# Performance work log

Measured on AMD Instinct MI355X. Metric: run time of the kernel, lower is better.

Reference implementation:

```python
import jax, jax.numpy as jnp
import numpy as np

N, E, D, ED, G = 50000, 800000, 64, 32, 50


def setup_inputs() -> dict:
    key = jax.random.key(0)
    ks = jax.random.split(key, 24)
    s = 0.05
    inp = {
        "x": jax.random.normal(ks[0], (N, D), jnp.float32),
        "edge_attr": jax.random.normal(ks[1], (E, ED), jnp.float32),
        "edge_index": jax.random.randint(ks[2], (2, E), 0, N, jnp.int64),
    }
    i = 3
    for step in range(2):
        inp[f"fe{step}_W1"] = jax.random.normal(ks[i], (2 * D + ED, D), jnp.float32) * s; i += 1
        inp[f"fe{step}_b1"] = jnp.zeros((D,), jnp.float32)
        inp[f"fe{step}_W2"] = jax.random.normal(ks[i], (D, D), jnp.float32) * s; i += 1
        inp[f"fe{step}_b2"] = jnp.zeros((D,), jnp.float32)
        inp[f"lstm{step}_Wih"] = jax.random.normal(ks[i], (D, 4 * D), jnp.float32) * s; i += 1
        inp[f"lstm{step}_Whh"] = jax.random.normal(ks[i], (D, 4 * D), jnp.float32) * s; i += 1
        inp[f"lstm{step}_bih"] = jnp.zeros((4 * D,), jnp.float32)
        inp[f"lstm{step}_bhh"] = jnp.zeros((4 * D,), jnp.float32)
    inp["gm_W"] = jax.random.normal(ks[i], (D, G), jnp.float32) * s; i += 1
    inp["gm_b"] = jnp.zeros((G,), jnp.float32)
    inp["fm_W"] = jax.random.normal(ks[i], (D, G), jnp.float32) * s; i += 1
    inp["fm_b"] = jnp.zeros((G,), jnp.float32)
    return inp


def _mpn(x, edge_attr, src, dst, W1, b1, W2, b2):
    # x_i = x[dst] (target), x_j = x[src] (source); aggregate 'add' at dst
    m = jnp.concatenate([x[dst], x[src], edge_attr], axis=1)  # [E, 2D+ED]
    m = jax.nn.relu(m @ W1 + b1) @ W2 + b2                    # [E, D]
    return jax.ops.segment_sum(m, dst, num_segments=x.shape[0])


def _lstm_cell(inp, h, c, Wih, Whh, bih, bhh):
    gates = inp @ Wih + h @ Whh + (bih + bhh)  # [N, 4D], gate order i,f,g,o
    i, f, g, o = jnp.split(gates, 4, axis=1)
    c = jax.nn.sigmoid(f) * c + jax.nn.sigmoid(i) * jnp.tanh(g)
    h = jax.nn.sigmoid(o) * jnp.tanh(c)
    return h, c


def reference(x, edge_attr, edge_index,
              fe0_W1, fe0_b1, fe0_W2, fe0_b2,
              lstm0_Wih, lstm0_Whh, lstm0_bih, lstm0_bhh,
              fe1_W1, fe1_b1, fe1_W2, fe1_b2,
              lstm1_Wih, lstm1_Whh, lstm1_bih, lstm1_bhh,
              gm_W, gm_b, fm_W, fm_b):
    src, dst = edge_index[0], edge_index[1]
    c = jnp.zeros_like(x)
    fes = [(fe0_W1, fe0_b1, fe0_W2, fe0_b2), (fe1_W1, fe1_b1, fe1_W2, fe1_b2)]
    lstms = [(lstm0_Wih, lstm0_Whh, lstm0_bih, lstm0_bhh),
             (lstm1_Wih, lstm1_Whh, lstm1_bih, lstm1_bhh)]
    for step in range(2):
        a = _mpn(x, edge_attr, src, dst, *fes[step])
        # LSTMCell(input=x, (h=a, c=c)) as in the original forward
        x, c = _lstm_cell(x, a, c, *lstms[step])
    g = jax.nn.sigmoid(x @ gm_W + gm_b)   # [N, G]
    h_v_G = x @ fm_W + fm_b               # [N, G]
    return jnp.sum(g * h_v_G, axis=0)     # [G]
```

## Files before the change

kernel.cpp:

```cpp
#include <hip/hip_runtime.h>
#include <hip/hip_bf16.h>

using short8 = __attribute__((ext_vector_type(8))) short;
using f32x4  = __attribute__((ext_vector_type(4))) float;

#define KLP 136

__device__ __forceinline__ unsigned short f2bf(float f) {
  unsigned u = __float_as_uint(f);
  u += 0x7FFFu + ((u >> 16) & 1u);
  return (unsigned short)(u >> 16);
}
__device__ __forceinline__ unsigned pack2(float a, float b) {
  return (unsigned)f2bf(a) | ((unsigned)f2bf(b) << 16);
}
#if __has_builtin(__builtin_amdgcn_rcpf)
__device__ __forceinline__ float fast_rcp(float x) { return __builtin_amdgcn_rcpf(x); }
#else
__device__ __forceinline__ float fast_rcp(float x) { return 1.f / x; }
#endif
__device__ __forceinline__ float sigm(float x) { return fast_rcp(1.f + __expf(-x)); }
__device__ __forceinline__ float tanh_f(float x) { return fmaf(2.f, sigm(2.f * x), -1.f); }

__global__ __launch_bounds__(256) void prep_all(
    const float* __restrict__ x,
    const float* __restrict__ W1_0, const float* __restrict__ Wih0,
    const float* __restrict__ bih0, const float* __restrict__ bhh0,
    const float* __restrict__ W1_1, const float* __restrict__ Wih1,
    const float* __restrict__ bih1, const float* __restrict__ bhh1,
    const float* __restrict__ W2_0, const float* __restrict__ Whh0, const float* __restrict__ b2_0,
    const float* __restrict__ W2_1, const float* __restrict__ Whh1, const float* __restrict__ b2_1,
    const float* __restrict__ gmW, const float* __restrict__ fmW,
    unsigned short* __restrict__ W1T,
    unsigned short* __restrict__ WcT,
    float* __restrict__ bG,
    float* __restrict__ b2h,
    unsigned short* __restrict__ WrT,
    unsigned short* __restrict__ xb0,
    float* __restrict__ aggrH,
    int* __restrict__ histA,
    float* __restrict__ outZ, int nOut,
    int N)
{
  int t = blockIdx.x * 256 + threadIdx.x;

  const int R0 = 2 * 26880 + 8192;
  if (t < R0) {
    const int per = 26880;
    if (t >= 2 * per) {
      int r2 = t - 2 * per;
      int o = r2 >> 6, k = r2 & 63;
      float v = 0.f;
      if (o < 50) v = gmW[k * 50 + o];
      else if (o >= 64 && o < 114) v = fmW[k * 50 + (o - 64)];
      WrT[o * 64 + k] = f2bf(v);
      return;
    }
    int step = t / per, r = t % per;
    const float* W1  = step ? W1_1 : W1_0;
    const float* Wih = step ? Wih1 : Wih0;
    const float* bih = step ? bih1 : bih0;
    const float* bhh = step ? bhh1 : bhh0;
    if (r < 10240) {
      int o = r / 160, k = r % 160;
      W1T[step * 10240 + o * 160 + k] = f2bf(W1[k * 64 + o]);
    } else if (r < 26624) {
      int rr = r - 10240;
      int g = rr >> 6, k = rr & 63;
      WcT[step * 32768 + g * 128 + k] = f2bf(Wih[k * 256 + g]);
    } else {
      int g = r - 26624;
      bG[step * 256 + g] = bih[g] + bhh[g];
    }
    return;
  }
  t -= R0;

  const int R1 = 33280;
  if (t < R1) {
    if (t < 32768) {
      int step = t >> 14, r = t & 16383;
      int g = r >> 6, k = r & 63;
      const float* W2  = step ? W2_1 : W2_0;
      const float* Whh = step ? Whh1 : Whh0;
      float v = 0.f;
      for (int j = 0; j < 64; ++j) v = fmaf(W2[k * 64 + j], Whh[j * 256 + g], v);
      WcT[step * 32768 + g * 128 + 64 + k] = f2bf(v);
    } else {
      int r = t - 32768;
      int step = r >> 8, g = r & 255;
      const float* b2  = step ? b2_1 : b2_0;
      const float* Whh = step ? Whh1 : Whh0;
      float v = 0.f;
      for (int j = 0; j < 64; ++j) v = fmaf(b2[j], Whh[j * 256 + g], v);
      b2h[step * 256 + g] = v;
    }
    return;
  }
  t -= R1;

  const int R2 = N * 8;
  if (t < R2) {
    const float4* p = (const float4*)(x + (long long)t * 8);
    float4 a0 = p[0], a1 = p[1];
    *(uint4*)(xb0 + (long long)t * 8) =
        make_uint4(pack2(a0.x, a0.y), pack2(a0.z, a0.w), pack2(a1.x, a1.y), pack2(a1.z, a1.w));
    return;
  }
  t -= R2;

  const int R3 = N * 16;
  if (t < R3) { ((float4*)aggrH)[t] = make_float4(0.f, 0.f, 0.f, 0.f); return; }
  t -= R3;

  const int R4 = N / 4;
  if (t < R4) { ((int4*)histA)[t] = make_int4(0, 0, 0, 0); return; }
  t -= R4;

  if (t < nOut) outZ[t] = 0.f;
}

__global__ __launch_bounds__(256) void hist_kernel(
    const int* __restrict__ dstI, int* __restrict__ hist, int E)
{
  int e = blockIdx.x * 256 + threadIdx.x;
  if (e < E) atomicAdd(&hist[dstI[e]], 1);
}

__global__ __launch_bounds__(256) void scan_part(
    const int* __restrict__ hist, int2* __restrict__ blockTot, int N)
{
  __shared__ int sD[256], sS[256];
  int t = threadIdx.x;
  int n = blockIdx.x * 256 + t;
  int d = (n < N) ? hist[n] : 0;
  int sg = (d + 15) >> 4;
  sD[t] = d; sS[t] = sg;
  __syncthreads();
  #pragma unroll
  for (int off = 128; off; off >>= 1) {
    if (t < off) { sD[t] += sD[t + off]; sS[t] += sS[t + off]; }
    __syncthreads();
  }
  if (t == 0) blockTot[blockIdx.x] = make_int2(sD[0], sS[0]);
}

__global__ __launch_bounds__(256) void scan_mid(
    const int2* __restrict__ blockTot, int2* __restrict__ blockBase,
    int* __restrict__ nSegTot, int nb)
{
  __shared__ int sD[256], sS[256];
  int t = threadIdx.x;
  int d = 0, s = 0;
  if (t < nb) { int2 v = blockTot[t]; d = v.x; s = v.y; }
  sD[t] = d; sS[t] = s;
  __syncthreads();
  #pragma unroll
  for (int off = 1; off < 256; off <<= 1) {
    int vd = (t >= off) ? sD[t - off] : 0;
    int vs = (t >= off) ? sS[t - off] : 0;
    __syncthreads();
    sD[t] += vd; sS[t] += vs;
    __syncthreads();
  }
  if (t < nb) blockBase[t] = make_int2(sD[t] - d, sS[t] - s);
  if (t == nb - 1) *nSegTot = sS[t];
}

__global__ __launch_bounds__(256) void scan_final(
    const int* __restrict__ hist, const int2* __restrict__ blockBase,
    int* __restrict__ cursor, int4* __restrict__ segInfo, int N)
{
  __shared__ int sD[256], sS[256];
  int t = threadIdx.x;
  int n = blockIdx.x * 256 + t;
  int d = (n < N) ? hist[n] : 0;
  int sg = (d + 15) >> 4;
  sD[t] = d; sS[t] = sg;
  __syncthreads();
  #pragma unroll
  for (int off = 1; off < 256; off <<= 1) {
    int vd = (t >= off) ? sD[t - off] : 0;
    int vs = (t >= off) ? sS[t - off] : 0;
    __syncthreads();
    sD[t] += vd; sS[t] += vs;
    __syncthreads();
  }
  if (n < N) {
    int2 bb = blockBase[blockIdx.x];
    int degBase = bb.x + sD[t] - d;
    int segBase = bb.y + sS[t] - sg;
    cursor[n] = degBase;
    for (int j = 0; j < sg; ++j)
      segInfo[segBase + j] = make_int4(degBase + j * 16, n, min(d - j * 16, 16), 0);
  }
}

__global__ __launch_bounds__(256) void scatter_perm(
    const int* __restrict__ srcI, const int* __restrict__ dstI,
    const float* __restrict__ ea, int* __restrict__ cursor,
    int* __restrict__ srcS, unsigned short* __restrict__ eaS, int E)
{
  const int t = threadIdx.x;
  const int l = t & 63;
  const int e = blockIdx.x * 64 + (t >> 2);
  const int c = t & 3;
  if (e >= E) return;
  int p = 0;
  if (c == 0) {
    int d = dstI[e];
    p = atomicAdd(&cursor[d], 1);
    srcS[p] = srcI[e];
  }
  p = __shfl(p, l & ~3);
  const float4* pe = (const float4*)(ea + (long long)e * 32 + c * 8);
  float4 a0 = pe[0], a1 = pe[1];
  *(uint4*)(eaS + (long long)p * 32 + c * 8) =
      make_uint4(pack2(a0.x, a0.y), pack2(a0.z, a0.w), pack2(a1.x, a1.y), pack2(a1.z, a1.w));
}

__global__ __launch_bounds__(256) void edge_gemm(
    const unsigned short* __restrict__ xb,
    const unsigned short* __restrict__ eaS,
    const int* __restrict__ srcS,
    const int4* __restrict__ segInfo,
    const int* __restrict__ nSegPtr,
    const unsigned short* __restrict__ W1T,
    const float* __restrict__ b1,
    float* __restrict__ aggrH)
{
  __shared__ unsigned short stash[20 * 64 * 8];
  const int t = threadIdx.x;
  const int w = t >> 6, l = t & 63;
  const int quad = l >> 4, lr = l & 15;

  #pragma unroll
  for (int p = 0; p < 5; ++p) {
    int idx = p * 256 + t;
    int grp = idx >> 6, ll = idx & 63;
    int kc = grp >> 2, n = grp & 3;
    *(uint4*)(stash + idx * 8) =
        *(const uint4*)(W1T + (n * 16 + (ll & 15)) * 160 + kc * 32 + (ll >> 4) * 8);
  }
  float bb[4];
  #pragma unroll
  for (int n = 0; n < 4; ++n) bb[n] = b1[n * 16 + lr];
  __syncthreads();

  const int nSeg = *nSegPtr;
  const int W = gridDim.x * 4;
  int s = blockIdx.x * 4 + w;
  if (s >= nSeg) return;
  int4 si = segInfo[s];
  int src = srcS[si.x + min(lr, si.z - 1)];

  while (true) {
    const int sn = s + W;
    const bool more = sn < nSeg;
    int4 si_n = si;
    if (more) si_n = segInfo[sn];

    const int start = si.x, node = si.y, cnt = si.z;
    const int er = min(lr, cnt - 1);

    const short8* pd = (const short8*)(xb + (long long)node * 64);
    const short8* ps = (const short8*)(xb + (long long)src * 64);
    short8 a0 = pd[quad];
    short8 a1 = pd[4 + quad];
    short8 a2 = ps[quad];
    short8 a3 = ps[4 + quad];
    short8 a4 = *(const short8*)(eaS + (long long)(start + er) * 32 + quad * 8);

    int src_n = src;
    if (more) src_n = srcS[si_n.x + min(lr, si_n.z - 1)];

    f32x4 acc[4] = {};
    #pragma unroll
    for (int kc = 0; kc < 5; ++kc) {
      short8 aX = (kc == 0) ? a0 : (kc == 1) ? a1 : (kc == 2) ? a2 : (kc == 3) ? a3 : a4;
      #pragma unroll
      for (int n = 0; n < 4; ++n) {
        short8 bFr = *(const short8*)(stash + (((kc << 2) | n) * 64 + l) * 8);
        acc[n] = __builtin_amdgcn_mfma_f32_16x16x32_bf16(aX, bFr, acc[n], 0, 0, 0);
      }
    }

    float myv = 0.f;
    #pragma unroll
    for (int n = 0; n < 4; ++n) {
      float sum = 0.f;
      #pragma unroll
      for (int rr = 0; rr < 4; ++rr) {
        float v = fmaxf(acc[n][rr] + bb[n], 0.f);
        sum += (quad * 4 + rr < cnt) ? v : 0.f;
      }
      sum += __shfl_xor(sum, 16);
      sum += __shfl_xor(sum, 32);
      if (quad == n) myv = sum;
    }
    unsafeAtomicAdd(&aggrH[(long long)node * 64 + l], myv);

    if (!more) break;
    s = sn; si = si_n; src = src_n;
  }
}

__global__ __launch_bounds__(256) void lstm3(
    const unsigned short* __restrict__ xbin,
    float* __restrict__ aggrH,
    const float* __restrict__ cin,
    float* __restrict__ cout,
    const unsigned short* __restrict__ WcT,
    const float* __restrict__ bG,
    const float* __restrict__ b2h,
    const int* __restrict__ degA,
    unsigned short* __restrict__ xbout,
    const unsigned short* __restrict__ WrT,
    const float* __restrict__ gb, const float* __restrict__ fb,
    float* __restrict__ outG,
    int nNodes, int zeroAggr, int doReadout)
{
  __shared__ unsigned short sIn[64 * KLP];
  __shared__ unsigned short sW[128 * 72];
  __shared__ float sBG[256], sB2h[256];
  const int t = threadIdx.x;
  sBG[t] = bG[t];
  sB2h[t] = b2h[t];

  const int base_n = blockIdx.x * 64;
  const int nl = t >> 2, q = t & 3;
  const int node = base_n + nl;
  unsigned short* rowp = sIn + nl * KLP;
  if (node < nNodes) {
    const uint4* px = (const uint4*)(xbin + (long long)node * 64);
    *(uint4*)(rowp + q * 16)     = px[q * 2];
    *(uint4*)(rowp + q * 16 + 8) = px[q * 2 + 1];
    float4* pg = (float4*)(aggrH + (long long)node * 64) + q * 4;
    float4 g0 = pg[0], g1 = pg[1], g2 = pg[2], g3 = pg[3];
    *(uint4*)(rowp + 64 + q * 16) =
        make_uint4(pack2(g0.x, g0.y), pack2(g0.z, g0.w), pack2(g1.x, g1.y), pack2(g1.z, g1.w));
    *(uint4*)(rowp + 64 + q * 16 + 8) =
        make_uint4(pack2(g2.x, g2.y), pack2(g2.z, g2.w), pack2(g3.x, g3.y), pack2(g3.z, g3.w));
    if (zeroAggr) {
      float4 z = make_float4(0.f, 0.f, 0.f, 0.f);
      pg[0] = z; pg[1] = z; pg[2] = z; pg[3] = z;
    }
  } else {
    *(uint4*)(rowp + q * 16)          = make_uint4(0, 0, 0, 0);
    *(uint4*)(rowp + q * 16 + 8)      = make_uint4(0, 0, 0, 0);
    *(uint4*)(rowp + 64 + q * 16)     = make_uint4(0, 0, 0, 0);
    *(uint4*)(rowp + 64 + q * 16 + 8) = make_uint4(0, 0, 0, 0);
  }

  const int w = t >> 6, l = t & 63, quad = l >> 4, lr = l & 15;
  const int row0 = w * 16;
  f32x4 acc[16] = {};
  for (int grp = 0; grp < 4; ++grp) {
    const uint4* gw = (const uint4*)WcT + (long long)(grp * 64) * 16;
    uint4* lw = (uint4*)sW;
    {
      int o0 = t >> 4, s4 = t & 15;
      #pragma unroll
      for (int pp = 0; pp < 4; ++pp) {
        int o = pp * 16 + o0;
        lw[o * 17 + s4] = gw[o * 16 + s4];
      }
    }
    __syncthreads();
    #pragma unroll
    for (int kc = 0; kc < 4; ++kc) {
      short8 aF = *(const short8*)(sIn + (row0 + lr) * KLP + kc * 32 + quad * 8);
      #pragma unroll
      for (int nt = 0; nt < 4; ++nt) {
        short8 bF = *(const short8*)(sW + (nt * 16 + lr) * KLP + kc * 32 + quad * 8);
        acc[grp * 4 + nt] = __builtin_amdgcn_mfma_f32_16x16x32_bf16(aF, bF, acc[grp * 4 + nt], 0, 0, 0);
      }
    }
    __syncthreads();
  }

  #pragma unroll
  for (int nt = 0; nt < 4; ++nt) {
    #pragma unroll
    for (int rr = 0; rr < 4; ++rr) {
      int node2 = base_n + row0 + quad * 4 + rr;
      int rl = row0 + quad * 4 + rr;
      int col = nt * 16 + lr;
      if (node2 < nNodes) {
        long long off = (long long)node2 * 64 + col;
        float dg = (float)degA[node2];
        float iv = acc[nt][rr]      + sBG[col]       + dg * sB2h[col];
        float fv = acc[4 + nt][rr]  + sBG[64 + col]  + dg * sB2h[64 + col];
        float gv = acc[8 + nt][rr]  + sBG[128 + col] + dg * sB2h[128 + col];
        float ov = acc[12 + nt][rr] + sBG[192 + col] + dg * sB2h[192 + col];
        float cOld = cin ? cin[off] : 0.f;
        float cN = sigm(fv) * cOld + sigm(iv) * tanh_f(gv);
        float hN = sigm(ov) * tanh_f(cN);
        if (doReadout) {
          sIn[rl * 72 + col] = f2bf(hN);
        } else {
          cout[off] = cN;
          xbout[off] = f2bf(hN);
        }
      } else if (doReadout) {
        sIn[rl * 72 + col] = 0;
      }
    }
  }

  if (!doReadout) return;

  __syncthreads();
  {
    const uint4* gw = (const uint4*)WrT;
    uint4* lw = (uint4*)sW;
    #pragma unroll
    for (int pp = 0; pp < 4; ++pp) {
      int idx = t + pp * 256;
      int o = idx >> 3, s = idx & 7;
      lw[o * 9 + s] = gw[idx];
    }
  }
  if (t < 64) {
    sBG[t]      = (t < 50) ? gb[t] : 0.f;
    sBG[64 + t] = (t < 50) ? fb[t] : 0.f;
  }
  __syncthreads();

  f32x4 racc[8] = {};
  #pragma unroll
  for (int kc = 0; kc < 2; ++kc) {
    short8 aF = *(const short8*)(sIn + (w * 16 + lr) * 72 + kc * 32 + quad * 8);
    #pragma unroll
    for (int n = 0; n < 8; ++n) {
      short8 bF = *(const short8*)(sW + (n * 16 + lr) * 72 + kc * 32 + quad * 8);
      racc[n] = __builtin_amdgcn_mfma_f32_16x16x32_bf16(aF, bF, racc[n], 0, 0, 0);
    }
  }
  float* sOutF = sB2h;
  #pragma unroll
  for (int n = 0; n < 4; ++n) {
    float val = 0.f;
    #pragma unroll
    for (int rr = 0; rr < 4; ++rr) {
      int nd = base_n + w * 16 + quad * 4 + rr;
      if (nd < nNodes) {
        int jj = n * 16 + lr;
        float gv = sigm(racc[n][rr] + sBG[jj]);
        float fv = racc[n + 4][rr] + sBG[64 + jj];
        val += gv * fv;
      }
    }
    val += __shfl_xor(val, 16);
    val += __shfl_xor(val, 32);
    if (quad == 0) sOutF[w * 64 + n * 16 + lr] = val;
  }
  __syncthreads();
  if (t < 50) {
    float sm = sOutF[t] + sOutF[64 + t] + sOutF[128 + t] + sOutF[192 + t];
    unsafeAtomicAdd(&outG[t], sm);
  }
}

extern "C" void kernel_launch(void* const* d_in, const int* in_sizes, int n_in,
                              void* d_out, int out_size, void* d_ws, size_t ws_size,
                              hipStream_t stream)
{
  const float* x      = (const float*)d_in[0];
  const float* ea     = (const float*)d_in[1];
  const int*   ei     = (const int*)d_in[2];
  const float* fe0_W1 = (const float*)d_in[3];
  const float* fe0_b1 = (const float*)d_in[4];
  const float* fe0_W2 = (const float*)d_in[5];
  const float* fe0_b2 = (const float*)d_in[6];
  const float* l0_Wih = (const float*)d_in[7];
  const float* l0_Whh = (const float*)d_in[8];
  const float* l0_bih = (const float*)d_in[9];
  const float* l0_bhh = (const float*)d_in[10];
  const float* fe1_W1 = (const float*)d_in[11];
  const float* fe1_b1 = (const float*)d_in[12];
  const float* fe1_W2 = (const float*)d_in[13];
  const float* fe1_b2 = (const float*)d_in[14];
  const float* l1_Wih = (const float*)d_in[15];
  const float* l1_Whh = (const float*)d_in[16];
  const float* l1_bih = (const float*)d_in[17];
  const float* l1_bhh = (const float*)d_in[18];
  const float* gm_W   = (const float*)d_in[19];
  const float* gm_b   = (const float*)d_in[20];
  const float* fm_W   = (const float*)d_in[21];
  const float* fm_b   = (const float*)d_in[22];

  const int N = in_sizes[0] / 64;
  const int E = in_sizes[1] / 32;
  const int* srcI = ei;
  const int* dstI = ei + E;

  char* ws = (char*)d_ws;
  unsigned short* xb0     = (unsigned short*)(ws + 0);
  unsigned short* xb1     = (unsigned short*)(ws + 6400000);
  float*          aggrH   = (float*)(ws + 12800000);
  float*          cbuf    = (float*)(ws + 25600000);
  unsigned short* eaS     = (unsigned short*)(ws + 38400000);
  int*            srcS    = (int*)(ws + 89601024);
  int4*           segInfo = (int4*)(ws + 92801088);
  int*            histA   = (int*)(ws + 94401280);
  int*            curA    = (int*)(ws + 94601280);
  unsigned short* W1T     = (unsigned short*)(ws + 94801280);
  unsigned short* WcT     = (unsigned short*)(ws + 94842240);
  float*          bG      = (float*)(ws + 94973312);
  float*          b2h     = (float*)(ws + 94975360);
  unsigned short* WrT     = (unsigned short*)(ws + 94977408);
  int*            nSegPtr = (int*)(ws + 94993792);
  int2*           blockTot  = (int2*)(ws + 94993856);
  int2*           blockBase = (int2*)(ws + 94995904);

  const int prepT = (2 * 26880 + 8192) + 33280 + N * 8 + N * 16 + N / 4 + out_size;
  prep_all<<<(prepT + 255) / 256, 256, 0, stream>>>(
      x,
      fe0_W1, l0_Wih, l0_bih, l0_bhh,
      fe1_W1, l1_Wih, l1_bih, l1_bhh,
      fe0_W2, l0_Whh, fe0_b2,
      fe1_W2, l1_Whh, fe1_b2,
      gm_W, fm_W,
      W1T, WcT, bG, b2h, WrT, xb0,
      aggrH, histA, (float*)d_out, out_size, N);

  const int nb = (N + 255) / 256;
  hist_kernel<<<(E + 255) / 256, 256, 0, stream>>>(dstI, histA, E);
  scan_part<<<nb, 256, 0, stream>>>(histA, blockTot, N);
  scan_mid<<<1, 256, 0, stream>>>(blockTot, blockBase, nSegPtr, nb);
  scan_final<<<nb, 256, 0, stream>>>(histA, blockBase, curA, segInfo, N);
  scatter_perm<<<(E + 63) / 64, 256, 0, stream>>>(srcI, dstI, ea, curA, srcS, eaS, E);

  const int nodeBlocks = (N + 63) / 64;

  edge_gemm<<<2048, 256, 0, stream>>>(xb0, eaS, srcS, segInfo, nSegPtr,
                                      W1T, fe0_b1, aggrH);
  lstm3<<<nodeBlocks, 256, 0, stream>>>(xb0, aggrH, nullptr, cbuf, WcT, bG, b2h,
                                        histA, xb1, WrT, gm_b, fm_b, (float*)d_out,
                                        N, 1, 0);

  edge_gemm<<<2048, 256, 0, stream>>>(xb1, eaS, srcS, segInfo, nSegPtr,
                                      W1T + 10240, fe1_b1, aggrH);
  lstm3<<<nodeBlocks, 256, 0, stream>>>(xb1, aggrH, cbuf, nullptr, WcT + 32768,
                                        bG + 256, b2h + 256, histA, nullptr,
                                        WrT, gm_b, fm_b, (float*)d_out,
                                        N, 0, 1);
}
```

Baseline: 435.1 us.

## Pre-convert edge attributes to bf16 in prep and hold two W1 chunks in registers

Moves the fp32-to-bf16 conversion of edge_attr out of scatter_perm and into the prep_all kernel, writing a contiguous bf16 copy that scatter_perm then permutes with plain 16-byte copies. In edge_gemm, the B fragments for the first two K chunks of W1 now stay in registers and only three chunks are staged through LDS, which cuts LDS traffic and shrinks the shared buffer. The trade-offs are an extra full pass that writes and rereads a bf16 edge buffer, and higher register pressure in edge_gemm.

```diff
diff --git a/kernel.cpp b/kernel.cpp
--- a/kernel.cpp
+++ b/kernel.cpp
@@ -24,6 +24,7 @@
 
 __global__ __launch_bounds__(256) void prep_all(
     const float* __restrict__ x,
+    const float* __restrict__ ea,
     const float* __restrict__ W1_0, const float* __restrict__ Wih0,
     const float* __restrict__ bih0, const float* __restrict__ bhh0,
     const float* __restrict__ W1_1, const float* __restrict__ Wih1,
@@ -37,10 +38,11 @@
     float* __restrict__ b2h,
     unsigned short* __restrict__ WrT,
     unsigned short* __restrict__ xb0,
+    unsigned short* __restrict__ eaB,
     float* __restrict__ aggrH,
     int* __restrict__ histA,
     float* __restrict__ outZ, int nOut,
-    int N)
+    int N, int E4)
 {
   int t = blockIdx.x * 256 + threadIdx.x;
 
@@ -117,7 +119,15 @@
   if (t < R4) { ((int4*)histA)[t] = make_int4(0, 0, 0, 0); return; }
   t -= R4;
 
-  if (t < nOut) outZ[t] = 0.f;
+  if (t < nOut) { outZ[t] = 0.f; return; }
+  t -= nOut;
+
+  if (t < E4) {
+    const float4* p = (const float4*)(ea + (long long)t * 8);
+    float4 a0 = p[0], a1 = p[1];
+    *(uint4*)(eaB + (long long)t * 8) =
+        make_uint4(pack2(a0.x, a0.y), pack2(a0.z, a0.w), pack2(a1.x, a1.y), pack2(a1.z, a1.w));
+  }
 }
 
 __global__ __launch_bounds__(256) void hist_kernel(
@@ -198,7 +208,7 @@
 
 __global__ __launch_bounds__(256) void scatter_perm(
     const int* __restrict__ srcI, const int* __restrict__ dstI,
-    const float* __restrict__ ea, int* __restrict__ cursor,
+    const unsigned short* __restrict__ eaB, int* __restrict__ cursor,
     int* __restrict__ srcS, unsigned short* __restrict__ eaS, int E)
 {
   const int t = threadIdx.x;
@@ -213,10 +223,8 @@
     srcS[p] = srcI[e];
   }
   p = __shfl(p, l & ~3);
-  const float4* pe = (const float4*)(ea + (long long)e * 32 + c * 8);
-  float4 a0 = pe[0], a1 = pe[1];
-  *(uint4*)(eaS + (long long)p * 32 + c * 8) =
-      make_uint4(pack2(a0.x, a0.y), pack2(a0.z, a0.w), pack2(a1.x, a1.y), pack2(a1.z, a1.w));
+  uint4 v = *(const uint4*)(eaB + (long long)e * 32 + c * 8);
+  *(uint4*)(eaS + (long long)p * 32 + c * 8) = v;
 }
 
 __global__ __launch_bounds__(256) void edge_gemm(
@@ -229,16 +237,23 @@
     const float* __restrict__ b1,
     float* __restrict__ aggrH)
 {
-  __shared__ unsigned short stash[20 * 64 * 8];
+  __shared__ unsigned short stash[12 * 64 * 8];
   const int t = threadIdx.x;
   const int w = t >> 6, l = t & 63;
   const int quad = l >> 4, lr = l & 15;
 
-  #pragma unroll
-  for (int p = 0; p < 5; ++p) {
+  short8 bF01[2][4];
+  #pragma unroll
+  for (int kc = 0; kc < 2; ++kc)
+    #pragma unroll
+    for (int n = 0; n < 4; ++n)
+      bF01[kc][n] = *(const short8*)(W1T + (n * 16 + lr) * 160 + kc * 32 + quad * 8);
+
+  #pragma unroll
+  for (int p = 0; p < 3; ++p) {
     int idx = p * 256 + t;
     int grp = idx >> 6, ll = idx & 63;
-    int kc = grp >> 2, n = grp & 3;
+    int kc = 2 + (grp >> 2), n = grp & 3;
     *(uint4*)(stash + idx * 8) =
         *(const uint4*)(W1T + (n * 16 + (ll & 15)) * 160 + kc * 32 + (ll >> 4) * 8);
   }
@@ -280,7 +295,9 @@
       short8 aX = (kc == 0) ? a0 : (kc == 1) ? a1 : (kc == 2) ? a2 : (kc == 3) ? a3 : a4;
       #pragma unroll
       for (int n = 0; n < 4; ++n) {
-        short8 bFr = *(const short8*)(stash + (((kc << 2) | n) * 64 + l) * 8);
+        short8 bFr = (kc < 2)
+            ? bF01[kc][n]
+            : *(const short8*)(stash + (((((kc - 2) << 2)) | n) * 64 + l) * 8);
         acc[n] = __builtin_amdgcn_mfma_f32_16x16x32_bf16(aX, bFr, acc[n], 0, 0, 0);
       }
     }
@@ -513,24 +530,26 @@
   int*            nSegPtr = (int*)(ws + 94993792);
   int2*           blockTot  = (int2*)(ws + 94993856);
   int2*           blockBase = (int2*)(ws + 94995904);
-
-  const int prepT = (2 * 26880 + 8192) + 33280 + N * 8 + N * 16 + N / 4 + out_size;
+  unsigned short* eaB     = (unsigned short*)(ws + 100000000);
+
+  const int E4 = E * 4;
+  const int prepT = (2 * 26880 + 8192) + 33280 + N * 8 + N * 16 + N / 4 + out_size + E4;
   prep_all<<<(prepT + 255) / 256, 256, 0, stream>>>(
-      x,
+      x, ea,
       fe0_W1, l0_Wih, l0_bih, l0_bhh,
       fe1_W1, l1_Wih, l1_bih, l1_bhh,
       fe0_W2, l0_Whh, fe0_b2,
       fe1_W2, l1_Whh, fe1_b2,
       gm_W, fm_W,
-      W1T, WcT, bG, b2h, WrT, xb0,
-      aggrH, histA, (float*)d_out, out_size, N);
+      W1T, WcT, bG, b2h, WrT, xb0, eaB,
+      aggrH, histA, (float*)d_out, out_size, N, E4);
 
   const int nb = (N + 255) / 256;
   hist_kernel<<<(E + 255) / 256, 256, 0, stream>>>(dstI, histA, E);
   scan_part<<<nb, 256, 0, stream>>>(histA, blockTot, N);
   scan_mid<<<1, 256, 0, stream>>>(blockTot, blockBase, nSegPtr, nb);
   scan_final<<<nb, 256, 0, stream>>>(histA, blockBase, curA, segInfo, N);
-  scatter_perm<<<(E + 63) / 64, 256, 0, stream>>>(srcI, dstI, ea, curA, srcS, eaS, E);
+  scatter_perm<<<(E + 63) / 64, 256, 0, stream>>>(srcI, dstI, eaB, curA, srcS, eaS, E);
 
   const int nodeBlocks = (N + 63) / 64;
 
```

After: 477.6 us. +9.8%, slower.

## Precompute per-destination-node W1 projection and reuse it as edge bias

Applied to the files above, without the earlier changes.

Adds a dst_gemm kernel that computes x[dst] @ W1_dst + b1 once per node and stores it in fp32. The edge kernel then skips the two dst K-chunks and adds that precomputed value as a per-segment bias, so it loads the bias instead of the dst node features. This drops 2 of 5 MFMA K-chunks per edge tile and shrinks the weight stash in LDS. The cost is one extra small kernel launch per step plus a 12.8MB fp32 write and read, and the dst term now stays in fp32 instead of being accumulated in the MFMA.

```diff
diff --git a/kernel.cpp b/kernel.cpp
--- a/kernel.cpp
+++ b/kernel.cpp
@@ -219,6 +219,60 @@
       make_uint4(pack2(a0.x, a0.y), pack2(a0.z, a0.w), pack2(a1.x, a1.y), pack2(a1.z, a1.w));
 }
 
+__global__ __launch_bounds__(256) void dst_gemm(
+    const unsigned short* __restrict__ xb,
+    const unsigned short* __restrict__ W1T,
+    const float* __restrict__ b1,
+    float* __restrict__ D,
+    int nNodes)
+{
+  __shared__ unsigned short sX[64 * 72];
+  const int t = threadIdx.x;
+  const int base = blockIdx.x * 64;
+  const int nl = t >> 2, q = t & 3;
+  const int node = base + nl;
+  {
+    uint4* dst = (uint4*)(sX + nl * 72 + q * 16);
+    if (node < nNodes) {
+      const uint4* px = (const uint4*)(xb + (long long)node * 64);
+      dst[0] = px[q * 2];
+      dst[1] = px[q * 2 + 1];
+    } else {
+      dst[0] = make_uint4(0, 0, 0, 0);
+      dst[1] = make_uint4(0, 0, 0, 0);
+    }
+  }
+  const int w = t >> 6, l = t & 63, quad = l >> 4, lr = l & 15;
+  short8 bF[2][4];
+  #pragma unroll
+  for (int kc = 0; kc < 2; ++kc)
+    #pragma unroll
+    for (int n = 0; n < 4; ++n)
+      bF[kc][n] = *(const short8*)(W1T + (n * 16 + lr) * 160 + kc * 32 + quad * 8);
+  float bb[4];
+  #pragma unroll
+  for (int n = 0; n < 4; ++n) bb[n] = b1[n * 16 + lr];
+  __syncthreads();
+
+  f32x4 acc[4] = {};
+  #pragma unroll
+  for (int kc = 0; kc < 2; ++kc) {
+    short8 aF = *(const short8*)(sX + (w * 16 + lr) * 72 + kc * 32 + quad * 8);
+    #pragma unroll
+    for (int n = 0; n < 4; ++n)
+      acc[n] = __builtin_amdgcn_mfma_f32_16x16x32_bf16(aF, bF[kc][n], acc[n], 0, 0, 0);
+  }
+  #pragma unroll
+  for (int n = 0; n < 4; ++n) {
+    #pragma unroll
+    for (int rr = 0; rr < 4; ++rr) {
+      int nd = base + w * 16 + quad * 4 + rr;
+      if (nd < nNodes)
+        D[(long long)nd * 64 + n * 16 + lr] = acc[n][rr] + bb[n];
+    }
+  }
+}
+
 __global__ __launch_bounds__(256) void edge_gemm(
     const unsigned short* __restrict__ xb,
     const unsigned short* __restrict__ eaS,
@@ -226,25 +280,22 @@
     const int4* __restrict__ segInfo,
     const int* __restrict__ nSegPtr,
     const unsigned short* __restrict__ W1T,
-    const float* __restrict__ b1,
+    const float* __restrict__ D,
     float* __restrict__ aggrH)
 {
-  __shared__ unsigned short stash[20 * 64 * 8];
+  __shared__ unsigned short stash[12 * 64 * 8];
   const int t = threadIdx.x;
   const int w = t >> 6, l = t & 63;
   const int quad = l >> 4, lr = l & 15;
 
   #pragma unroll
-  for (int p = 0; p < 5; ++p) {
+  for (int p = 0; p < 3; ++p) {
     int idx = p * 256 + t;
     int grp = idx >> 6, ll = idx & 63;
-    int kc = grp >> 2, n = grp & 3;
+    int kc = 2 + (grp >> 2), n = grp & 3;
     *(uint4*)(stash + idx * 8) =
         *(const uint4*)(W1T + (n * 16 + (ll & 15)) * 160 + kc * 32 + (ll >> 4) * 8);
   }
-  float bb[4];
-  #pragma unroll
-  for (int n = 0; n < 4; ++n) bb[n] = b1[n * 16 + lr];
   __syncthreads();
 
   const int nSeg = *nSegPtr;
@@ -253,6 +304,11 @@
   if (s >= nSeg) return;
   int4 si = segInfo[s];
   int src = srcS[si.x + min(lr, si.z - 1)];
+  float Dv0, Dv1, Dv2, Dv3;
+  {
+    const float* dp = D + (long long)si.y * 64 + lr;
+    Dv0 = dp[0]; Dv1 = dp[16]; Dv2 = dp[32]; Dv3 = dp[48];
+  }
 
   while (true) {
     const int sn = s + W;
@@ -263,21 +319,23 @@
     const int start = si.x, node = si.y, cnt = si.z;
     const int er = min(lr, cnt - 1);
 
-    const short8* pd = (const short8*)(xb + (long long)node * 64);
     const short8* ps = (const short8*)(xb + (long long)src * 64);
-    short8 a0 = pd[quad];
-    short8 a1 = pd[4 + quad];
     short8 a2 = ps[quad];
     short8 a3 = ps[4 + quad];
     short8 a4 = *(const short8*)(eaS + (long long)(start + er) * 32 + quad * 8);
 
     int src_n = src;
-    if (more) src_n = srcS[si_n.x + min(lr, si_n.z - 1)];
+    float Dn0 = Dv0, Dn1 = Dv1, Dn2 = Dv2, Dn3 = Dv3;
+    if (more) {
+      src_n = srcS[si_n.x + min(lr, si_n.z - 1)];
+      const float* dp = D + (long long)si_n.y * 64 + lr;
+      Dn0 = dp[0]; Dn1 = dp[16]; Dn2 = dp[32]; Dn3 = dp[48];
+    }
 
     f32x4 acc[4] = {};
     #pragma unroll
-    for (int kc = 0; kc < 5; ++kc) {
-      short8 aX = (kc == 0) ? a0 : (kc == 1) ? a1 : (kc == 2) ? a2 : (kc == 3) ? a3 : a4;
+    for (int kc = 0; kc < 3; ++kc) {
+      short8 aX = (kc == 0) ? a2 : (kc == 1) ? a3 : a4;
       #pragma unroll
       for (int n = 0; n < 4; ++n) {
         short8 bFr = *(const short8*)(stash + (((kc << 2) | n) * 64 + l) * 8);
@@ -288,10 +346,11 @@
     float myv = 0.f;
     #pragma unroll
     for (int n = 0; n < 4; ++n) {
+      float bias = (n == 0) ? Dv0 : (n == 1) ? Dv1 : (n == 2) ? Dv2 : Dv3;
       float sum = 0.f;
       #pragma unroll
       for (int rr = 0; rr < 4; ++rr) {
-        float v = fmaxf(acc[n][rr] + bb[n], 0.f);
+        float v = fmaxf(acc[n][rr] + bias, 0.f);
         sum += (quad * 4 + rr < cnt) ? v : 0.f;
       }
       sum += __shfl_xor(sum, 16);
@@ -302,6 +361,7 @@
 
     if (!more) break;
     s = sn; si = si_n; src = src_n;
+    Dv0 = Dn0; Dv1 = Dn1; Dv2 = Dn2; Dv3 = Dn3;
   }
 }
 
@@ -513,6 +573,7 @@
   int*            nSegPtr = (int*)(ws + 94993792);
   int2*           blockTot  = (int2*)(ws + 94993856);
   int2*           blockBase = (int2*)(ws + 94995904);
+  float*          Dbuf    = (float*)(ws + 96000000);
 
   const int prepT = (2 * 26880 + 8192) + 33280 + N * 8 + N * 16 + N / 4 + out_size;
   prep_all<<<(prepT + 255) / 256, 256, 0, stream>>>(
@@ -534,14 +595,16 @@
 
   const int nodeBlocks = (N + 63) / 64;
 
+  dst_gemm<<<nodeBlocks, 256, 0, stream>>>(xb0, W1T, fe0_b1, Dbuf, N);
   edge_gemm<<<2048, 256, 0, stream>>>(xb0, eaS, srcS, segInfo, nSegPtr,
-                                      W1T, fe0_b1, aggrH);
+                                      W1T, Dbuf, aggrH);
   lstm3<<<nodeBlocks, 256, 0, stream>>>(xb0, aggrH, nullptr, cbuf, WcT, bG, b2h,
                                         histA, xb1, WrT, gm_b, fm_b, (float*)d_out,
                                         N, 1, 0);
 
+  dst_gemm<<<nodeBlocks, 256, 0, stream>>>(xb1, W1T + 10240, fe1_b1, Dbuf, N);
   edge_gemm<<<2048, 256, 0, stream>>>(xb1, eaS, srcS, segInfo, nSegPtr,
-                                      W1T + 10240, fe1_b1, aggrH);
+                                      W1T + 10240, Dbuf, aggrH);
   lstm3<<<nodeBlocks, 256, 0, stream>>>(xb1, aggrH, cbuf, nullptr, WcT + 32768,
                                         bG + 256, b2h + 256, histA, nullptr,
                                         WrT, gm_b, fm_b, (float*)d_out,
```

Measured after the change: 424.3 us. 1.03x faster.
